# Kernel tuning notes

Measured on AMD Instinct MI355X. Metric: run time of the kernel, lower is better.

The kernel has to match this reference:

```python
import jax, jax.numpy as jnp
import numpy as np

N, N_OBS, D, HID = 200000, 100000, 32, 128

def setup_inputs() -> dict:
    key = jax.random.key(0)
    ks = jax.random.split(key, 24)
    p = lambda k, shp: jax.random.normal(k, shp, dtype=jnp.float32) * 0.05
    inp = {
        "current_time": jnp.ones((1, 1), dtype=jnp.float32),
        "mgn_h": jax.random.normal(ks[0], (N, HID), dtype=jnp.float32),
        "X_obs": jax.random.normal(ks[1], (N_OBS, D), dtype=jnp.float32),
        "M_obs": (jax.random.uniform(ks[2], (N_OBS, D)) < 0.5).astype(jnp.float32),
        "i_obs": jnp.arange(N_OBS, dtype=jnp.int32),  # unique, in-range row ids
        "last_x": jax.random.normal(ks[3], (N, D), dtype=jnp.float32),
        "last_t": jax.random.uniform(ks[4], (N, D), dtype=jnp.float32),
        "W_gx": p(ks[5], (D, D)),
        "W_gh": p(ks[6], (HID, D)),
        "Wz": p(ks[7], (D, HID)), "Vz": p(ks[8], (D, HID)), "Uz": p(ks[9], (HID, HID)), "bz": jnp.zeros((HID,), jnp.float32),
        "Wr": p(ks[10], (D, HID)), "Vr": p(ks[11], (D, HID)), "Ur": p(ks[12], (HID, HID)), "br": jnp.zeros((HID,), jnp.float32),
        "Wh": p(ks[13], (D, HID)), "Vh": p(ks[14], (D, HID)), "Uh": p(ks[15], (HID, HID)), "bh": jnp.zeros((HID,), jnp.float32),
    }
    return inp


def reference(current_time, mgn_h, X_obs, M_obs, i_obs, last_x, last_t,
              W_gx, W_gh, Wz, Vz, Uz, bz, Wr, Vr, Ur, br, Wh, Vh, Uh, bh):
    # --- masked scatter update of last observed values ---
    last_x = last_x.at[i_obs].set(last_x[i_obs] * (1.0 - M_obs) + X_obs * M_obs)
    # mean over observed rows (faithful to original: numerator sums raw X_obs)
    mean_x = jnp.sum(X_obs, axis=0, keepdims=True) / jnp.sum(M_obs + 1e-6, axis=0, keepdims=True)
    interval = current_time - last_t                       # [N, D]
    last_t = last_t.at[i_obs].set(last_t[i_obs] * (1.0 - M_obs) + current_time * M_obs)
    # decay gates (torch Linear: x @ W.T, no bias)
    gamma_x = jnp.exp(-jax.nn.relu(interval @ W_gx.T))      # [N, D]
    gamma_h = jnp.exp(-jax.nn.relu(interval @ W_gh.T))      # [N, HID]
    gx = gamma_x[i_obs]                                     # [n_obs, D]
    X_hat = (M_obs * X_obs
             + (1.0 - M_obs) * gx * last_x[i_obs]
             + (1.0 - M_obs) * (1.0 - gx) * mean_x)
    # --- GRU-D cell on observed rows ---
    h = gamma_h[i_obs] * mgn_h[i_obs]                       # decayed hidden [n_obs, HID]
    z = jax.nn.sigmoid(X_hat @ Wz + M_obs @ Vz + h @ Uz + bz)
    r = jax.nn.sigmoid(X_hat @ Wr + M_obs @ Vr + h @ Ur + br)
    h_tilde = jnp.tanh(X_hat @ Wh + M_obs @ Vh + (r * h) @ Uh + bh)
    h_new = (1.0 - z) * h + z * h_tilde
    mgn_h = mgn_h.at[i_obs].set(h_new)
    return mgn_h, last_x, last_t
```

## Files before the change

### kernel.cpp

```cpp
#include <hip/hip_runtime.h>
#include <hip/hip_bf16.h>

#define D_ 32
#define HID_ 128
#define ROWS 32
#define NCOPY 1024
#define NB_Z 25
#define NB_P 308
#define NB_M 512

typedef __attribute__((ext_vector_type(8))) short bf16x8;
typedef __attribute__((ext_vector_type(4))) float f32x4;
typedef __attribute__((ext_vector_type(4))) unsigned short us4;

__device__ __forceinline__ unsigned short bfh(float v) {
    __hip_bfloat16 b = __float2bfloat16(v);
    unsigned short u;
    __builtin_memcpy(&u, &b, 2);
    return u;
}
__device__ __forceinline__ float bfh2f(unsigned short u) {
    return __uint_as_float(((unsigned)u) << 16);
}
__device__ __forceinline__ float fsig(float x) {
    return __fdividef(1.0f, 1.0f + __expf(-x));
}
__device__ __forceinline__ float ftanh(float x) {
    return 1.0f - __fdividef(2.0f, __expf(2.0f * x) + 1.0f);
}

__global__ __launch_bounds__(256) void kA(
    unsigned* __restrict__ bm, int nwords,
    const float* __restrict__ W_gx, const float* __restrict__ W_gh,
    const float* __restrict__ Wz, const float* __restrict__ Vz, const float* __restrict__ Uz,
    const float* __restrict__ Wr, const float* __restrict__ Vr, const float* __restrict__ Ur,
    const float* __restrict__ Wh, const float* __restrict__ Vh, const float* __restrict__ Uh,
    short* __restrict__ gxh, short* __restrict__ gxl,
    short* __restrict__ ghh, short* __restrict__ ghl,
    short* __restrict__ zrh, short* __restrict__ zrl,
    short* __restrict__ h3h, short* __restrict__ h3l,
    const float* __restrict__ X_obs, const float* __restrict__ M_obs,
    float* __restrict__ partials, int n_obs, int chunk)
{
    __shared__ float4 rx[32][9], rm[32][9];
    int bid = blockIdx.x;
    if (bid < NB_Z) {
        int i = bid * 256 + threadIdx.x;
        if (i < nwords) bm[i] = 0u;
        return;
    }
    if (bid < NB_Z + NB_P) {
        int tid = (bid - NB_Z) * 256 + threadIdx.x;
        if (tid >= 78848) return;
        float v = 0.f;
        short* ph;
        short* pl;
        int local;
        if (tid < 1024) {
            local = tid;
            int j = local & 7, lane = (local >> 3) & 63, tn = local >> 9;
            int k = ((lane >> 4) << 3) + j;
            int n = tn * 16 + (lane & 15);
            v = W_gx[n * D_ + k];
            ph = gxh; pl = gxl;
        } else if (tid < 5120) {
            local = tid - 1024;
            int j = local & 7, lane = (local >> 3) & 63, tn = local >> 9;
            int k = ((lane >> 4) << 3) + j;
            int n = tn * 16 + (lane & 15);
            v = W_gh[n * D_ + k];
            ph = ghh; pl = ghl;
        } else if (tid < 54272) {
            local = tid - 5120;
            int j = local & 7, lane = (local >> 3) & 63, fs = local >> 9;
            int ks = fs % 6, tn = fs / 6;
            int k = ks * 32 + ((lane >> 4) << 3) + j;
            int n = tn * 16 + (lane & 15);
            const float *W, *V, *U;
            int nc;
            if (n < 128) { W = Wz; V = Vz; U = Uz; nc = n; }
            else         { W = Wr; V = Vr; U = Ur; nc = n - 128; }
            if (k < 32)       v = W[k * HID_ + nc];
            else if (k < 64)  v = V[(k - 32) * HID_ + nc];
            else              v = U[(k - 64) * HID_ + nc];
            ph = zrh; pl = zrl;
        } else {
            local = tid - 54272;
            int j = local & 7, lane = (local >> 3) & 63, fs = local >> 9;
            int ks = fs % 6, tn = fs / 6;
            int k = ks * 32 + ((lane >> 4) << 3) + j;
            int n = tn * 16 + (lane & 15);
            if (k < 32)       v = Wh[k * HID_ + n];
            else if (k < 64)  v = Vh[(k - 32) * HID_ + n];
            else              v = Uh[(k - 64) * HID_ + n];
            ph = h3h; pl = h3l;
        }
        unsigned short hi = bfh(v);
        unsigned short lo = bfh(v - bfh2f(hi));
        ph[local] = (short)hi;
        pl[local] = (short)lo;
        return;
    }
    int mb = bid - (NB_Z + NB_P);
    int start = mb * chunk;
    int end = start + chunk;
    if (end > n_obs) end = n_obs;
    int rq = threadIdx.x >> 3, c4 = threadIdx.x & 7;
    float4 sx = make_float4(0.f, 0.f, 0.f, 0.f);
    float4 sm = sx;
    for (int j = start + rq; j < end; j += 32) {
        float4 xv = ((const float4*)X_obs)[j * 8 + c4];
        float4 mv = ((const float4*)M_obs)[j * 8 + c4];
        sx.x += xv.x; sx.y += xv.y; sx.z += xv.z; sx.w += xv.w;
        sm.x += mv.x + 1e-6f; sm.y += mv.y + 1e-6f; sm.z += mv.z + 1e-6f; sm.w += mv.w + 1e-6f;
    }
    rx[rq][c4] = sx;
    rm[rq][c4] = sm;
    __syncthreads();
    #pragma unroll
    for (int off = 16; off >= 1; off >>= 1) {
        if (rq < off) {
            float4 a = rx[rq][c4], b = rx[rq + off][c4];
            a.x += b.x; a.y += b.y; a.z += b.z; a.w += b.w;
            rx[rq][c4] = a;
            float4 c = rm[rq][c4], d = rm[rq + off][c4];
            c.x += d.x; c.y += d.y; c.z += d.z; c.w += d.w;
            rm[rq][c4] = c;
        }
        __syncthreads();
    }
    if (threadIdx.x < 8) {
        *(float4*)&partials[mb * 64 + threadIdx.x * 4]      = rx[0][threadIdx.x];
        *(float4*)&partials[mb * 64 + 32 + threadIdx.x * 4] = rm[0][threadIdx.x];
    }
}

__global__ __launch_bounds__(256) void kB(
    const int* __restrict__ i_obs, unsigned* __restrict__ bm, int n_obs, int nbB,
    const float* __restrict__ partials, float* __restrict__ mean_x)
{
    __shared__ float red[4][64];
    int bid = blockIdx.x;
    if (bid < nbB) {
        int i = bid * 256 + threadIdx.x;
        if (i < n_obs) {
            int gi = i_obs[i];
            atomicOr(&bm[gi >> 5], 1u << (gi & 31));
        }
        return;
    }
    int t = threadIdx.x;
    int s = t >> 6, d = t & 63;
    float acc = 0.f;
    for (int b = s; b < NB_M; b += 4) acc += partials[b * 64 + d];
    red[s][d] = acc;
    __syncthreads();
    if (t < 64) red[0][t] = red[0][t] + red[1][t] + red[2][t] + red[3][t];
    __syncthreads();
    if (t < 32) mean_x[t] = red[0][t] / red[0][t + 32];
}

__global__ __launch_bounds__(512, 8) void k_fused(
    const float* __restrict__ ct_p,
    const float* __restrict__ mgn_h,
    const float* __restrict__ X_obs,
    const float* __restrict__ M_obs,
    const int*   __restrict__ i_obs,
    const float* __restrict__ last_x,
    const float* __restrict__ last_t,
    const float* __restrict__ bz, const float* __restrict__ br, const float* __restrict__ bh,
    const float* __restrict__ mean_x,
    const short* __restrict__ gxh, const short* __restrict__ gxl,
    const short* __restrict__ ghh, const short* __restrict__ ghl,
    const short* __restrict__ zrh, const short* __restrict__ zrl,
    const short* __restrict__ h3h, const short* __restrict__ h3l,
    const unsigned* __restrict__ bm,
    float* __restrict__ out_h, float* __restrict__ out_lx, float* __restrict__ out_lt,
    int n_obs, int N, int nblk)
{
    __shared__ unsigned short sh_h_hi[ROWS][136], sh_h_lo[ROWS][136];
    __shared__ unsigned short sh_ivxh_hi[ROWS][40], sh_ivxh_lo[ROWS][40];
    __shared__ unsigned short sh_M[ROWS][40];
    __shared__ float s_lxn[ROWS][33];
    __shared__ float s_mean[D_];
    __shared__ int   s_idx[ROWS];

    const int t = threadIdx.x;
    const int bid = blockIdx.x;

    if (bid >= nblk) {
        int rid = bid - nblk;
        long nh = (long)N * (HID_ / 4);
        long nx = (long)N * (D_ / 4);
        long total = nh + 2 * nx;
        const float4* s_mgn_g = (const float4*)mgn_h;
        const float4* s_lx_g  = (const float4*)last_x;
        const float4* s_lt_g  = (const float4*)last_t;
        float4* d_h  = (float4*)out_h;
        float4* d_lx = (float4*)out_lx;
        float4* d_lt = (float4*)out_lt;
        for (long i = (long)rid * 512 + t; i < total; i += (long)NCOPY * 512) {
            if (i < nh) {
                int row = (int)(i >> 5);
                if (!((bm[row >> 5] >> (row & 31)) & 1u)) d_h[i] = s_mgn_g[i];
            } else if (i < nh + nx) {
                long j = i - nh;
                int row = (int)(j >> 3);
                if (!((bm[row >> 5] >> (row & 31)) & 1u)) d_lx[j] = s_lx_g[j];
            } else {
                long j = i - nh - nx;
                int row = (int)(j >> 3);
                if (!((bm[row >> 5] >> (row & 31)) & 1u)) d_lt[j] = s_lt_g[j];
            }
        }
        return;
    }

    const int row0 = bid * ROWS;
    const int wave = t >> 6, lane = t & 63;
    const int lo4 = lane & 15, hi2 = lane >> 4;

    if (t < ROWS) {
        int j = row0 + t;
        s_idx[t] = (j < n_obs) ? i_obs[j] : -1;
    }
    if (t >= 64 && t < 96) s_mean[t - 64] = mean_x[t - 64];
    __syncthreads();
    const float ctv = ct_p[0];

    float hreg[2][4];
    {
        int c = wave * 16 + lo4;
        #pragma unroll
        for (int si = 0; si < 2; si++) {
            #pragma unroll
            for (int q = 0; q < 4; q++) {
                int r = si * 16 + hi2 * 4 + q;
                int gi = s_idx[r];
                hreg[si][q] = (gi >= 0) ? mgn_h[(long)gi * HID_ + c] : 0.f;
            }
        }
    }

    if (t < 256) {
        int rr = t >> 3, c4 = t & 7, d0 = c4 * 4;
        int gi = s_idx[rr];
        float4 Mm = make_float4(0.f, 0.f, 0.f, 0.f);
        float4 itv = Mm, lxn = Mm;
        if (gi >= 0) {
            int j = row0 + rr;
            float4 Xv = ((const float4*)X_obs)[j * 8 + c4];
            Mm = ((const float4*)M_obs)[j * 8 + c4];
            float4 lx = ((const float4*)last_x)[(long)gi * 8 + c4];
            float4 lt = ((const float4*)last_t)[(long)gi * 8 + c4];
            float4 ltn;
            itv.x = ctv - lt.x; lxn.x = lx.x * (1.f - Mm.x) + Xv.x * Mm.x; ltn.x = lt.x * (1.f - Mm.x) + ctv * Mm.x;
            itv.y = ctv - lt.y; lxn.y = lx.y * (1.f - Mm.y) + Xv.y * Mm.y; ltn.y = lt.y * (1.f - Mm.y) + ctv * Mm.y;
            itv.z = ctv - lt.z; lxn.z = lx.z * (1.f - Mm.z) + Xv.z * Mm.z; ltn.z = lt.z * (1.f - Mm.z) + ctv * Mm.z;
            itv.w = ctv - lt.w; lxn.w = lx.w * (1.f - Mm.w) + Xv.w * Mm.w; ltn.w = lt.w * (1.f - Mm.w) + ctv * Mm.w;
            ((float4*)out_lx)[(long)gi * 8 + c4] = lxn;
            ((float4*)out_lt)[(long)gi * 8 + c4] = ltn;
        }
        us4 ih, il, mh;
        {
            unsigned short h0 = bfh(itv.x); ih.x = h0; il.x = bfh(itv.x - bfh2f(h0)); mh.x = bfh(Mm.x);
            unsigned short h1 = bfh(itv.y); ih.y = h1; il.y = bfh(itv.y - bfh2f(h1)); mh.y = bfh(Mm.y);
            unsigned short h2 = bfh(itv.z); ih.z = h2; il.z = bfh(itv.z - bfh2f(h2)); mh.z = bfh(Mm.z);
            unsigned short h3 = bfh(itv.w); ih.w = h3; il.w = bfh(itv.w - bfh2f(h3)); mh.w = bfh(Mm.w);
        }
        *(us4*)&sh_ivxh_hi[rr][d0] = ih;
        *(us4*)&sh_ivxh_lo[rr][d0] = il;
        *(us4*)&sh_M[rr][d0]       = mh;
        s_lxn[rr][d0 + 0] = lxn.x; s_lxn[rr][d0 + 1] = lxn.y; s_lxn[rr][d0 + 2] = lxn.z; s_lxn[rr][d0 + 3] = lxn.w;
    }
    __syncthreads();

    const bf16x8* vgxh = (const bf16x8*)gxh;
    const bf16x8* vgxl = (const bf16x8*)gxl;
    const bf16x8* vghh = (const bf16x8*)ghh;
    const bf16x8* vghl = (const bf16x8*)ghl;
    const bf16x8* vzrh = (const bf16x8*)zrh;
    const bf16x8* vzrl = (const bf16x8*)zrl;
    const bf16x8* vh3h = (const bf16x8*)h3h;
    const bf16x8* vh3l = (const bf16x8*)h3l;

    {
        bf16x8 bhi = vghh[wave * 64 + lane];
        bf16x8 blo = vghl[wave * 64 + lane];
        int c = wave * 16 + lo4;
        #pragma unroll
        for (int si = 0; si < 2; si++) {
            int ar = si * 16 + lo4;
            bf16x8 ahi = *(const bf16x8*)&sh_ivxh_hi[ar][hi2 * 8];
            bf16x8 alo = *(const bf16x8*)&sh_ivxh_lo[ar][hi2 * 8];
            f32x4 acc = {0.f, 0.f, 0.f, 0.f};
            acc = __builtin_amdgcn_mfma_f32_16x16x32_bf16(ahi, bhi, acc, 0, 0, 0);
            acc = __builtin_amdgcn_mfma_f32_16x16x32_bf16(ahi, blo, acc, 0, 0, 0);
            acc = __builtin_amdgcn_mfma_f32_16x16x32_bf16(alo, bhi, acc, 0, 0, 0);
            #pragma unroll
            for (int q = 0; q < 4; q++) {
                int r = si * 16 + hi2 * 4 + q;
                float g = __expf(-fmaxf(acc[q], 0.f));
                float hv = g * hreg[si][q];
                hreg[si][q] = hv;
                unsigned short hh = bfh(hv);
                sh_h_hi[r][c] = hh;
                sh_h_lo[r][c] = bfh(hv - bfh2f(hh));
            }
        }
    }
    f32x4 gxacc[2];
    if (wave < 2) {
        bf16x8 bhi = vgxh[wave * 64 + lane];
        bf16x8 blo = vgxl[wave * 64 + lane];
        #pragma unroll
        for (int si = 0; si < 2; si++) {
            int ar = si * 16 + lo4;
            bf16x8 ahi = *(const bf16x8*)&sh_ivxh_hi[ar][hi2 * 8];
            bf16x8 alo = *(const bf16x8*)&sh_ivxh_lo[ar][hi2 * 8];
            f32x4 acc = {0.f, 0.f, 0.f, 0.f};
            acc = __builtin_amdgcn_mfma_f32_16x16x32_bf16(ahi, bhi, acc, 0, 0, 0);
            acc = __builtin_amdgcn_mfma_f32_16x16x32_bf16(ahi, blo, acc, 0, 0, 0);
            acc = __builtin_amdgcn_mfma_f32_16x16x32_bf16(alo, bhi, acc, 0, 0, 0);
            gxacc[si] = acc;
        }
    }
    __syncthreads();

    if (wave < 2) {
        int c = wave * 16 + lo4;
        float mn2 = s_mean[c];
        #pragma unroll
        for (int si = 0; si < 2; si++) {
            #pragma unroll
            for (int q = 0; q < 4; q++) {
                int r = si * 16 + hi2 * 4 + q;
                float g = __expf(-fmaxf(gxacc[si][q], 0.f));
                float Mv = bfh2f(sh_M[r][c]);
                float lx = s_lxn[r][c];
                float xh = lx * (Mv + (1.f - Mv) * g) + (1.f - Mv) * (1.f - g) * mn2;
                unsigned short xhh = bfh(xh);
                sh_ivxh_hi[r][c] = xhh;
                sh_ivxh_lo[r][c] = bfh(xh - bfh2f(xhh));
            }
        }
    }
    __syncthreads();

    f32x4 accA[2][2];
    #pragma unroll
    for (int ti = 0; ti < 2; ti++)
        #pragma unroll
        for (int si = 0; si < 2; si++)
            accA[ti][si] = (f32x4){0.f, 0.f, 0.f, 0.f};

    #pragma unroll
    for (int ks = 0; ks < 6; ks++) {
        bf16x8 Ah[2], Al[2];
        bool hasLo = (ks != 1);
        #pragma unroll
        for (int si = 0; si < 2; si++) {
            int ar = si * 16 + lo4;
            if (ks == 0) {
                Ah[si] = *(const bf16x8*)&sh_ivxh_hi[ar][hi2 * 8];
                Al[si] = *(const bf16x8*)&sh_ivxh_lo[ar][hi2 * 8];
            } else if (ks == 1) {
                Ah[si] = *(const bf16x8*)&sh_M[ar][hi2 * 8];
                Al[si] = Ah[si];
            } else {
                int ko = (ks - 2) * 32 + hi2 * 8;
                Ah[si] = *(const bf16x8*)&sh_h_hi[ar][ko];
                Al[si] = *(const bf16x8*)&sh_h_lo[ar][ko];
            }
        }
        #pragma unroll
        for (int ti = 0; ti < 2; ti++) {
            int tn = wave + ti * 8;
            int slot = (tn * 6 + ks) * 64 + lane;
            bf16x8 bhi = vzrh[slot];
            bf16x8 blo = vzrl[slot];
            #pragma unroll
            for (int si = 0; si < 2; si++) {
                f32x4 a = accA[ti][si];
                a = __builtin_amdgcn_mfma_f32_16x16x32_bf16(Ah[si], bhi, a, 0, 0, 0);
                a = __builtin_amdgcn_mfma_f32_16x16x32_bf16(Ah[si], blo, a, 0, 0, 0);
                if (hasLo)
                    a = __builtin_amdgcn_mfma_f32_16x16x32_bf16(Al[si], bhi, a, 0, 0, 0);
                accA[ti][si] = a;
            }
        }
    }
    float zreg[2][4], rreg[2][4];
    {
        int c = wave * 16 + lo4;
        float bzv = bz[c], brv = br[c];
        #pragma unroll
        for (int si = 0; si < 2; si++)
            #pragma unroll
            for (int q = 0; q < 4; q++) {
                zreg[si][q] = fsig(accA[0][si][q] + bzv);
                rreg[si][q] = fsig(accA[1][si][q] + brv);
            }
    }
    __syncthreads();

    {
        int c = wave * 16 + lo4;
        #pragma unroll
        for (int si = 0; si < 2; si++) {
            #pragma unroll
            for (int q = 0; q < 4; q++) {
                int r = si * 16 + hi2 * 4 + q;
                float rh = rreg[si][q] * hreg[si][q];
                unsigned short rhh = bfh(rh);
                sh_h_hi[r][c] = rhh;
                sh_h_lo[r][c] = bfh(rh - bfh2f(rhh));
            }
        }
    }
    __syncthreads();

    f32x4 accB[2];
    #pragma unroll
    for (int si = 0; si < 2; si++)
        accB[si] = (f32x4){0.f, 0.f, 0.f, 0.f};

    #pragma unroll
    for (int ks = 0; ks < 6; ks++) {
        bf16x8 Ah[2], Al[2];
        bool hasLo = (ks != 1);
        #pragma unroll
        for (int si = 0; si < 2; si++) {
            int ar = si * 16 + lo4;
            if (ks == 0) {
                Ah[si] = *(const bf16x8*)&sh_ivxh_hi[ar][hi2 * 8];
                Al[si] = *(const bf16x8*)&sh_ivxh_lo[ar][hi2 * 8];
            } else if (ks == 1) {
                Ah[si] = *(const bf16x8*)&sh_M[ar][hi2 * 8];
                Al[si] = Ah[si];
            } else {
                int ko = (ks - 2) * 32 + hi2 * 8;
                Ah[si] = *(const bf16x8*)&sh_h_hi[ar][ko];
                Al[si] = *(const bf16x8*)&sh_h_lo[ar][ko];
            }
        }
        int slot = (wave * 6 + ks) * 64 + lane;
        bf16x8 bhi = vh3h[slot];
        bf16x8 blo = vh3l[slot];
        #pragma unroll
        for (int si = 0; si < 2; si++) {
            f32x4 a = accB[si];
            a = __builtin_amdgcn_mfma_f32_16x16x32_bf16(Ah[si], bhi, a, 0, 0, 0);
            a = __builtin_amdgcn_mfma_f32_16x16x32_bf16(Ah[si], blo, a, 0, 0, 0);
            if (hasLo)
                a = __builtin_amdgcn_mfma_f32_16x16x32_bf16(Al[si], bhi, a, 0, 0, 0);
            accB[si] = a;
        }
    }
    {
        int c = wave * 16 + lo4;
        float bhv = bh[c];
        #pragma unroll
        for (int si = 0; si < 2; si++) {
            #pragma unroll
            for (int q = 0; q < 4; q++) {
                int r = si * 16 + hi2 * 4 + q;
                int gi = s_idx[r];
                if (gi < 0) continue;
                float ht = ftanh(accB[si][q] + bhv);
                float z  = zreg[si][q];
                out_h[(long)gi * HID_ + c] = (1.f - z) * hreg[si][q] + z * ht;
            }
        }
    }
}

extern "C" void kernel_launch(void* const* d_in, const int* in_sizes, int n_in,
                              void* d_out, int out_size, void* d_ws, size_t ws_size,
                              hipStream_t stream)
{
    const float* ct     = (const float*)d_in[0];
    const float* mgn_h  = (const float*)d_in[1];
    const float* X_obs  = (const float*)d_in[2];
    const float* M_obs  = (const float*)d_in[3];
    const int*   i_obs  = (const int*)d_in[4];
    const float* last_x = (const float*)d_in[5];
    const float* last_t = (const float*)d_in[6];
    const float* W_gx   = (const float*)d_in[7];
    const float* W_gh   = (const float*)d_in[8];
    const float* Wz = (const float*)d_in[9];
    const float* Vz = (const float*)d_in[10];
    const float* Uz = (const float*)d_in[11];
    const float* bz = (const float*)d_in[12];
    const float* Wr = (const float*)d_in[13];
    const float* Vr = (const float*)d_in[14];
    const float* Ur = (const float*)d_in[15];
    const float* br = (const float*)d_in[16];
    const float* Wh = (const float*)d_in[17];
    const float* Vh = (const float*)d_in[18];
    const float* Uh = (const float*)d_in[19];
    const float* bh = (const float*)d_in[20];

    int n_obs = in_sizes[4];
    int N = in_sizes[1] / HID_;

    float* out_h  = (float*)d_out;
    float* out_lx = out_h + (long)N * HID_;
    float* out_lt = out_lx + (long)N * D_;

    char* w = (char*)d_ws;
    float* partials = (float*)w;
    float* mean_x   = (float*)(w + 131072);
    short* gxh = (short*)(w + 131200);
    short* gxl = (short*)(w + 133248);
    short* ghh = (short*)(w + 135296);
    short* ghl = (short*)(w + 143488);
    short* zrh = (short*)(w + 151680);
    short* zrl = (short*)(w + 249984);
    short* h3h = (short*)(w + 348288);
    short* h3l = (short*)(w + 397440);
    unsigned* bm = (unsigned*)(w + 446592);

    int nwords = (N + 31) / 32;
    int chunk = (n_obs + NB_M - 1) / NB_M;
    kA<<<NB_Z + NB_P + NB_M, 256, 0, stream>>>(
        bm, nwords,
        W_gx, W_gh, Wz, Vz, Uz, Wr, Vr, Ur, Wh, Vh, Uh,
        gxh, gxl, ghh, ghl, zrh, zrl, h3h, h3l,
        X_obs, M_obs, partials, n_obs, chunk);

    int nbB = (n_obs + 255) / 256;
    kB<<<nbB + 1, 256, 0, stream>>>(i_obs, bm, n_obs, nbB, partials, mean_x);

    int nblk = (n_obs + ROWS - 1) / ROWS;
    k_fused<<<nblk + NCOPY, 512, 0, stream>>>(
        ct, mgn_h, X_obs, M_obs, i_obs, last_x, last_t,
        bz, br, bh, mean_x,
        gxh, gxl, ghh, ghl, zrh, zrl, h3h, h3l,
        bm, out_h, out_lx, out_lt, n_obs, N, nblk);
}
```

Measured before the change: 158.6 us.

## Drop split-bf16 low-part activations and interleave copy blocks with compute blocks

Activation operands are now stored as a single bf16 instead of a hi/lo bf16 pair, which removes the third MFMA per tile along with the matching LDS stores and loads. Weights keep their hi/lo split. Separately, the block-id mapping is changed so that every fourth block is a copy block spread among the compute blocks, rather than all copy blocks sitting at the end of the grid. The precision cut lowers the accuracy of the interval, X_hat and h operands and may push results past tolerance.

```diff
diff --git a/kernel.cpp b/kernel.cpp
--- a/kernel.cpp
+++ b/kernel.cpp
@@ -178,8 +178,8 @@
     float* __restrict__ out_h, float* __restrict__ out_lx, float* __restrict__ out_lt,
     int n_obs, int N, int nblk)
 {
-    __shared__ unsigned short sh_h_hi[ROWS][136], sh_h_lo[ROWS][136];
-    __shared__ unsigned short sh_ivxh_hi[ROWS][40], sh_ivxh_lo[ROWS][40];
+    __shared__ unsigned short sh_h[ROWS][136];
+    __shared__ unsigned short sh_ivxh[ROWS][40];
     __shared__ unsigned short sh_M[ROWS][40];
     __shared__ float s_lxn[ROWS][33];
     __shared__ float s_mean[D_];
@@ -188,8 +188,17 @@
     const int t = threadIdx.x;
     const int bid = blockIdx.x;
 
-    if (bid >= nblk) {
-        int rid = bid - nblk;
+    bool isCopy = false;
+    int rid;
+    const int inter = 4 * NCOPY;
+    if (bid < inter) {
+        if ((bid & 3) == 3) { isCopy = true; rid = bid >> 2; }
+        else                {                rid = (bid >> 2) * 3 + (bid & 3); }
+    } else {
+        rid = 3 * NCOPY + (bid - inter);
+    }
+
+    if (isCopy) {
         long nh = (long)N * (HID_ / 4);
         long nx = (long)N * (D_ / 4);
         long total = nh + 2 * nx;
@@ -215,8 +224,9 @@
         }
         return;
     }
-
-    const int row0 = bid * ROWS;
+    if (rid >= nblk) return;
+
+    const int row0 = rid * ROWS;
     const int wave = t >> 6, lane = t & 63;
     const int lo4 = lane & 15, hi2 = lane >> 4;
 
@@ -261,16 +271,13 @@
             ((float4*)out_lx)[(long)gi * 8 + c4] = lxn;
             ((float4*)out_lt)[(long)gi * 8 + c4] = ltn;
         }
-        us4 ih, il, mh;
-        {
-            unsigned short h0 = bfh(itv.x); ih.x = h0; il.x = bfh(itv.x - bfh2f(h0)); mh.x = bfh(Mm.x);
-            unsigned short h1 = bfh(itv.y); ih.y = h1; il.y = bfh(itv.y - bfh2f(h1)); mh.y = bfh(Mm.y);
-            unsigned short h2 = bfh(itv.z); ih.z = h2; il.z = bfh(itv.z - bfh2f(h2)); mh.z = bfh(Mm.z);
-            unsigned short h3 = bfh(itv.w); ih.w = h3; il.w = bfh(itv.w - bfh2f(h3)); mh.w = bfh(Mm.w);
-        }
-        *(us4*)&sh_ivxh_hi[rr][d0] = ih;
-        *(us4*)&sh_ivxh_lo[rr][d0] = il;
-        *(us4*)&sh_M[rr][d0]       = mh;
+        us4 ih, mh;
+        ih.x = bfh(itv.x); mh.x = bfh(Mm.x);
+        ih.y = bfh(itv.y); mh.y = bfh(Mm.y);
+        ih.z = bfh(itv.z); mh.z = bfh(Mm.z);
+        ih.w = bfh(itv.w); mh.w = bfh(Mm.w);
+        *(us4*)&sh_ivxh[rr][d0] = ih;
+        *(us4*)&sh_M[rr][d0]    = mh;
         s_lxn[rr][d0 + 0] = lxn.x; s_lxn[rr][d0 + 1] = lxn.y; s_lxn[rr][d0 + 2] = lxn.z; s_lxn[rr][d0 + 3] = lxn.w;
     }
     __syncthreads();
@@ -291,21 +298,17 @@
         #pragma unroll
         for (int si = 0; si < 2; si++) {
             int ar = si * 16 + lo4;
-            bf16x8 ahi = *(const bf16x8*)&sh_ivxh_hi[ar][hi2 * 8];
-            bf16x8 alo = *(const bf16x8*)&sh_ivxh_lo[ar][hi2 * 8];
+            bf16x8 ahi = *(const bf16x8*)&sh_ivxh[ar][hi2 * 8];
             f32x4 acc = {0.f, 0.f, 0.f, 0.f};
             acc = __builtin_amdgcn_mfma_f32_16x16x32_bf16(ahi, bhi, acc, 0, 0, 0);
             acc = __builtin_amdgcn_mfma_f32_16x16x32_bf16(ahi, blo, acc, 0, 0, 0);
-            acc = __builtin_amdgcn_mfma_f32_16x16x32_bf16(alo, bhi, acc, 0, 0, 0);
             #pragma unroll
             for (int q = 0; q < 4; q++) {
                 int r = si * 16 + hi2 * 4 + q;
                 float g = __expf(-fmaxf(acc[q], 0.f));
                 float hv = g * hreg[si][q];
                 hreg[si][q] = hv;
-                unsigned short hh = bfh(hv);
-                sh_h_hi[r][c] = hh;
-                sh_h_lo[r][c] = bfh(hv - bfh2f(hh));
+                sh_h[r][c] = bfh(hv);
             }
         }
     }
@@ -316,12 +319,10 @@
         #pragma unroll
         for (int si = 0; si < 2; si++) {
             int ar = si * 16 + lo4;
-            bf16x8 ahi = *(const bf16x8*)&sh_ivxh_hi[ar][hi2 * 8];
-            bf16x8 alo = *(const bf16x8*)&sh_ivxh_lo[ar][hi2 * 8];
+            bf16x8 ahi = *(const bf16x8*)&sh_ivxh[ar][hi2 * 8];
             f32x4 acc = {0.f, 0.f, 0.f, 0.f};
             acc = __builtin_amdgcn_mfma_f32_16x16x32_bf16(ahi, bhi, acc, 0, 0, 0);
             acc = __builtin_amdgcn_mfma_f32_16x16x32_bf16(ahi, blo, acc, 0, 0, 0);
-            acc = __builtin_amdgcn_mfma_f32_16x16x32_bf16(alo, bhi, acc, 0, 0, 0);
             gxacc[si] = acc;
         }
     }
@@ -339,9 +340,7 @@
                 float Mv = bfh2f(sh_M[r][c]);
                 float lx = s_lxn[r][c];
                 float xh = lx * (Mv + (1.f - Mv) * g) + (1.f - Mv) * (1.f - g) * mn2;
-                unsigned short xhh = bfh(xh);
-                sh_ivxh_hi[r][c] = xhh;
-                sh_ivxh_lo[r][c] = bfh(xh - bfh2f(xhh));
+                sh_ivxh[r][c] = bfh(xh);
             }
         }
     }
@@ -356,22 +355,13 @@
 
     #pragma unroll
     for (int ks = 0; ks < 6; ks++) {
-        bf16x8 Ah[2], Al[2];
-        bool hasLo = (ks != 1);
+        bf16x8 Ah[2];
         #pragma unroll
         for (int si = 0; si < 2; si++) {
             int ar = si * 16 + lo4;
-            if (ks == 0) {
-                Ah[si] = *(const bf16x8*)&sh_ivxh_hi[ar][hi2 * 8];
-                Al[si] = *(const bf16x8*)&sh_ivxh_lo[ar][hi2 * 8];
-            } else if (ks == 1) {
-                Ah[si] = *(const bf16x8*)&sh_M[ar][hi2 * 8];
-                Al[si] = Ah[si];
-            } else {
-                int ko = (ks - 2) * 32 + hi2 * 8;
-                Ah[si] = *(const bf16x8*)&sh_h_hi[ar][ko];
-                Al[si] = *(const bf16x8*)&sh_h_lo[ar][ko];
-            }
+            if (ks == 0)      Ah[si] = *(const bf16x8*)&sh_ivxh[ar][hi2 * 8];
+            else if (ks == 1) Ah[si] = *(const bf16x8*)&sh_M[ar][hi2 * 8];
+            else              Ah[si] = *(const bf16x8*)&sh_h[ar][(ks - 2) * 32 + hi2 * 8];
         }
         #pragma unroll
         for (int ti = 0; ti < 2; ti++) {
@@ -384,8 +374,6 @@
                 f32x4 a = accA[ti][si];
                 a = __builtin_amdgcn_mfma_f32_16x16x32_bf16(Ah[si], bhi, a, 0, 0, 0);
                 a = __builtin_amdgcn_mfma_f32_16x16x32_bf16(Ah[si], blo, a, 0, 0, 0);
-                if (hasLo)
-                    a = __builtin_amdgcn_mfma_f32_16x16x32_bf16(Al[si], bhi, a, 0, 0, 0);
                 accA[ti][si] = a;
             }
         }
@@ -411,10 +399,7 @@
             #pragma unroll
             for (int q = 0; q < 4; q++) {
                 int r = si * 16 + hi2 * 4 + q;
-                float rh = rreg[si][q] * hreg[si][q];
-                unsigned short rhh = bfh(rh);
-                sh_h_hi[r][c] = rhh;
-                sh_h_lo[r][c] = bfh(rh - bfh2f(rhh));
+                sh_h[r][c] = bfh(rreg[si][q] * hreg[si][q]);
             }
         }
     }
@@ -427,22 +412,13 @@
 
     #pragma unroll
     for (int ks = 0; ks < 6; ks++) {
-        bf16x8 Ah[2], Al[2];
-        bool hasLo = (ks != 1);
+        bf16x8 Ah[2];
         #pragma unroll
         for (int si = 0; si < 2; si++) {
             int ar = si * 16 + lo4;
-            if (ks == 0) {
-                Ah[si] = *(const bf16x8*)&sh_ivxh_hi[ar][hi2 * 8];
-                Al[si] = *(const bf16x8*)&sh_ivxh_lo[ar][hi2 * 8];
-            } else if (ks == 1) {
-                Ah[si] = *(const bf16x8*)&sh_M[ar][hi2 * 8];
-                Al[si] = Ah[si];
-            } else {
-                int ko = (ks - 2) * 32 + hi2 * 8;
-                Ah[si] = *(const bf16x8*)&sh_h_hi[ar][ko];
-                Al[si] = *(const bf16x8*)&sh_h_lo[ar][ko];
-            }
+            if (ks == 0)      Ah[si] = *(const bf16x8*)&sh_ivxh[ar][hi2 * 8];
+            else if (ks == 1) Ah[si] = *(const bf16x8*)&sh_M[ar][hi2 * 8];
+            else              Ah[si] = *(const bf16x8*)&sh_h[ar][(ks - 2) * 32 + hi2 * 8];
         }
         int slot = (wave * 6 + ks) * 64 + lane;
         bf16x8 bhi = vh3h[slot];
@@ -452,8 +428,6 @@
             f32x4 a = accB[si];
             a = __builtin_amdgcn_mfma_f32_16x16x32_bf16(Ah[si], bhi, a, 0, 0, 0);
             a = __builtin_amdgcn_mfma_f32_16x16x32_bf16(Ah[si], blo, a, 0, 0, 0);
-            if (hasLo)
-                a = __builtin_amdgcn_mfma_f32_16x16x32_bf16(Al[si], bhi, a, 0, 0, 0);
             accB[si] = a;
         }
     }
@@ -533,7 +507,8 @@
     kB<<<nbB + 1, 256, 0, stream>>>(i_obs, bm, n_obs, nbB, partials, mean_x);
 
     int nblk = (n_obs + ROWS - 1) / ROWS;
-    k_fused<<<nblk + NCOPY, 512, 0, stream>>>(
+    int grid = (nblk > 3 * NCOPY) ? (nblk + NCOPY) : (4 * NCOPY);
+    k_fused<<<grid, 512, 0, stream>>>(
         ct, mgn_h, X_obs, M_obs, i_obs, last_x, last_t,
         bz, br, bh, mean_x,
         gxh, gxl, ghh, ghl, zrh, zrl, h3h, h3l,
```

Result: faster. 153.0 us (-3.5%).
